# Performance work log

Measured on AMD Instinct MI355X. Metric: run time of the kernel, lower is better.

## Reference

```python
import jax, jax.numpy as jnp
import numpy as np

RANK = 32
ALPHA = 1.0
SCALE = ALPHA / RANK


def setup_inputs() -> dict:
    key = jax.random.key(0)
    k1, k2, k3, k4, k5 = jax.random.split(key, 5)
    B_, S, D_in, D_out = 4, 2048, 4096, 4096
    x = jax.random.normal(k1, (B_, S, D_in), dtype=jnp.float32)
    # nn.Linear weight: [out, in], kaiming-ish scale
    W = jax.random.normal(k2, (D_out, D_in), dtype=jnp.float32) / np.sqrt(D_in)
    bias = jax.random.normal(k3, (D_out,), dtype=jnp.float32) * 0.01
    A = jax.random.normal(k4, (D_in, RANK), dtype=jnp.float32) * 0.01
    # torch init is zeros for B; use small random so output depends on LoRA path
    Bm = jax.random.normal(k5, (RANK, D_out), dtype=jnp.float32) * 0.01
    return {"x": x, "W": W, "bias": bias, "A": A, "B": Bm}


def reference(x, W, bias, A, B):
    # Original: y = x @ (W + scale*(A@B)^T)^T + bias
    # Mathematically identical fused form (two GEMMs, no [in,out] delta):
    base = jnp.einsum('bsd,od->bso', x, W)          # [B,S,out]
    lora = jnp.einsum('bsr,ro->bso', x @ A, B)       # [B,S,rank]->[B,S,out]
    return base + SCALE * lora + bias
```

## Files before the change

kernel.cpp:

```cpp
#include <hip/hip_runtime.h>
#include <hip/hip_bf16.h>
#include <stdint.h>

#define RANK 32
#define SCALE (1.0f / 32.0f)

typedef __bf16 bf16x8 __attribute__((ext_vector_type(8)));
typedef float f32x4 __attribute__((ext_vector_type(4)));

__device__ __forceinline__ void gload16(const void* g, void* l) {
  __builtin_amdgcn_global_load_lds(
      (const __attribute__((address_space(1))) unsigned int*)g,
      (__attribute__((address_space(3))) unsigned int*)l, 16, 0, 0);
}

__device__ __forceinline__ unsigned short f2bf(float f) {
  __hip_bfloat16 h = __float2bfloat16(f);
  return *reinterpret_cast<unsigned short*>(&h);
}

__global__ __launch_bounds__(256) void transpose_B_k(const float* __restrict__ B,
                                                     float* __restrict__ Bt,
                                                     int Dout) {
  int idx = blockIdx.x * 256 + threadIdx.x;
  int r = idx / Dout;
  int o = idx - r * Dout;
  Bt[(long long)o * RANK + r] = B[idx];
}

__global__ __launch_bounds__(256) void merge_W_k(const float* __restrict__ W,
                                                 const float* __restrict__ A,
                                                 const float* __restrict__ Bt,
                                                 unsigned short* __restrict__ Wb,
                                                 int Din, int Dout) {
  __shared__ float sB[16 * RANK];
  int nib = Din / 256;
  int ib = blockIdx.x % nib;
  int ob = blockIdx.x / nib;
  int i0 = ib * 256, o0 = ob * 16;
  int t = threadIdx.x;

  if (t < 128) {
    reinterpret_cast<float4*>(sB)[t] =
        reinterpret_cast<const float4*>(Bt + (long long)o0 * RANK)[t];
  }

  float a[RANK];
  const float4* Ap = reinterpret_cast<const float4*>(A + (long long)(i0 + t) * RANK);
#pragma unroll
  for (int c = 0; c < RANK / 4; ++c) {
    float4 v = Ap[c];
    a[c * 4 + 0] = v.x; a[c * 4 + 1] = v.y;
    a[c * 4 + 2] = v.z; a[c * 4 + 3] = v.w;
  }
  __syncthreads();

  for (int o = 0; o < 16; ++o) {
    float d = 0.f;
#pragma unroll
    for (int j = 0; j < RANK; ++j) d += a[j] * sB[o * RANK + j];
    long long off = (long long)(o0 + o) * Din + i0 + t;
    Wb[off] = f2bf(W[off] + SCALE * d);
  }
}

__global__ __launch_bounds__(256) void cast_x_k(const float* __restrict__ in,
                                                unsigned short* __restrict__ out,
                                                long long n8) {
  long long i = (long long)blockIdx.x * 256 + threadIdx.x;
  if (i >= n8) return;
  const float4* in4 = reinterpret_cast<const float4*>(in) + i * 2;
  float4 v0 = in4[0], v1 = in4[1];
  union { unsigned short u[8]; uint4 q; } p;
  p.u[0] = f2bf(v0.x); p.u[1] = f2bf(v0.y); p.u[2] = f2bf(v0.z); p.u[3] = f2bf(v0.w);
  p.u[4] = f2bf(v1.x); p.u[5] = f2bf(v1.y); p.u[6] = f2bf(v1.z); p.u[7] = f2bf(v1.w);
  reinterpret_cast<uint4*>(out)[i] = p.q;
}

template <int NISSUE>
__device__ __forceinline__ void stage(const unsigned short* g, int K, int koff,
                                      int row0, unsigned short* ldsbase,
                                      int t, int wid) {
  int r = t >> 3;
  int cg = (t & 7) ^ (r & 7);
#pragma unroll
  for (int i = 0; i < NISSUE; ++i) {
    gload16(g + (long long)(row0 + i * 64 + r) * K + koff + cg * 8,
            ldsbase + (row0 + i * 64) * 64 + wid * 512);
  }
}

__device__ __forceinline__ int swz_off(int rowl, int k) {
  return rowl * 64 + ((((k) >> 3) ^ (rowl & 7)) << 3);
}

__global__ __launch_bounds__(512, 2) void gemm256_bias_k(
    const unsigned short* __restrict__ Xb,
    const unsigned short* __restrict__ Wb,
    const float* __restrict__ bias,
    float* __restrict__ Out,
    int M, int N, int K) {
  __shared__ unsigned short As[2][256 * 64];
  __shared__ unsigned short Bs[2][256 * 64];

  int nbn = N / 256;
  int cpx = gridDim.x >> 3;
  int bid = blockIdx.x;
  int swz = (bid & 7) * cpx + (bid >> 3);
  int bm = swz / nbn, bn = swz % nbn;

  int t = threadIdx.x;
  int wid = t >> 6, lane = t & 63;
  int wr = wid >> 2, wc = wid & 3;
  int lr = lane & 15, kq = (lane >> 4) * 8;
  int aw = wr * 128, bw = wc * 64;

  const unsigned short* ga = Xb + (long long)bm * 256 * K;
  const unsigned short* gb = Wb + (long long)bn * 256 * K;

  f32x4 acc[8][4] = {};
  bf16x8 a[4][2], b0[2][2], b0n[2][2], b1[2][2];

  const int NT = K / 64;

#define LDA(BUF, ROFF, MM, KS) \
  (*(const bf16x8*)&As[BUF][swz_off(aw + (ROFF) + (MM) * 16 + lr, (KS) * 32 + kq)])
#define LDB(BUF, ROFF, NN, KS) \
  (*(const bf16x8*)&Bs[BUF][swz_off(bw + (ROFF) + (NN) * 16 + lr, (KS) * 32 + kq)])

  stage<4>(ga, K, 0, 0, &As[0][0], t, wid);
  stage<4>(gb, K, 0, 0, &Bs[0][0], t, wid);
  stage<4>(ga, K, 64, 0, &As[1][0], t, wid);
  asm volatile("s_waitcnt vmcnt(4)" ::: "memory");
  __builtin_amdgcn_s_barrier();
#pragma unroll
  for (int m = 0; m < 4; ++m) {
    a[m][0] = LDA(0, 0, m, 0); a[m][1] = LDA(0, 0, m, 1);
  }
#pragma unroll
  for (int n = 0; n < 2; ++n) {
    b0[n][0] = LDB(0, 0, n, 0);  b0[n][1] = LDB(0, 0, n, 1);
    b1[n][0] = LDB(0, 32, n, 0); b1[n][1] = LDB(0, 32, n, 1);
  }

  for (int kt = 0; kt < NT; ++kt) {
    const int cur = kt & 1;
    int konext = (kt + 1) * 64, konext2 = (kt + 2) * 64;
    const bool hasN = (kt + 1 < NT);

    if (hasN) stage<2>(gb, K, konext, 0, &Bs[cur ^ 1][0], t, wid);
    __builtin_amdgcn_s_setprio(1);
#pragma unroll
    for (int m = 0; m < 4; ++m)
#pragma unroll
      for (int n = 0; n < 2; ++n)
#pragma unroll
        for (int ks = 0; ks < 2; ++ks)
          acc[m][n] = __builtin_amdgcn_mfma_f32_16x16x32_bf16(a[m][ks], b0[n][ks], acc[m][n], 0, 0, 0);
    __builtin_amdgcn_s_setprio(0);
    __builtin_amdgcn_s_barrier();

    if (hasN) stage<2>(gb, K, konext, 128, &Bs[cur ^ 1][0], t, wid);
    __builtin_amdgcn_s_setprio(1);
#pragma unroll
    for (int m = 0; m < 4; ++m) {
      acc[m][2] = __builtin_amdgcn_mfma_f32_16x16x32_bf16(a[m][0], b1[0][0], acc[m][2], 0, 0, 0);
      acc[m][2] = __builtin_amdgcn_mfma_f32_16x16x32_bf16(a[m][1], b1[0][1], acc[m][2], 0, 0, 0);
      acc[m][3] = __builtin_amdgcn_mfma_f32_16x16x32_bf16(a[m][0], b1[1][0], acc[m][3], 0, 0, 0);
      acc[m][3] = __builtin_amdgcn_mfma_f32_16x16x32_bf16(a[m][1], b1[1][1], acc[m][3], 0, 0, 0);
      a[m][0] = LDA(cur, 64, m, 0);
      a[m][1] = LDA(cur, 64, m, 1);
    }
    __builtin_amdgcn_s_setprio(0);
    __builtin_amdgcn_s_barrier();

    __builtin_amdgcn_s_setprio(1);
#pragma unroll
    for (int m = 0; m < 4; ++m)
#pragma unroll
      for (int n = 0; n < 2; ++n)
#pragma unroll
        for (int ks = 0; ks < 2; ++ks)
          acc[4 + m][2 + n] = __builtin_amdgcn_mfma_f32_16x16x32_bf16(a[m][ks], b1[n][ks], acc[4 + m][2 + n], 0, 0, 0);
    __builtin_amdgcn_s_setprio(0);
    __builtin_amdgcn_s_barrier();

    if (kt + 2 < NT) {
      stage<4>(ga, K, konext2, 0, &As[cur][0], t, wid);
      asm volatile("s_waitcnt vmcnt(4)" ::: "memory");
    } else if (hasN) {
      asm volatile("s_waitcnt vmcnt(0)" ::: "memory");
    }
    __builtin_amdgcn_s_barrier();

    if (hasN) {
      b0n[0][0] = LDB(cur ^ 1, 0, 0, 0); b0n[0][1] = LDB(cur ^ 1, 0, 0, 1);
      b0n[1][0] = LDB(cur ^ 1, 0, 1, 0); b0n[1][1] = LDB(cur ^ 1, 0, 1, 1);
    }
    __builtin_amdgcn_s_setprio(1);
#pragma unroll
    for (int m = 0; m < 4; ++m) {
      acc[4 + m][0] = __builtin_amdgcn_mfma_f32_16x16x32_bf16(a[m][0], b0[0][0], acc[4 + m][0], 0, 0, 0);
      acc[4 + m][0] = __builtin_amdgcn_mfma_f32_16x16x32_bf16(a[m][1], b0[0][1], acc[4 + m][0], 0, 0, 0);
      acc[4 + m][1] = __builtin_amdgcn_mfma_f32_16x16x32_bf16(a[m][0], b0[1][0], acc[4 + m][1], 0, 0, 0);
      acc[4 + m][1] = __builtin_amdgcn_mfma_f32_16x16x32_bf16(a[m][1], b0[1][1], acc[4 + m][1], 0, 0, 0);
      if (hasN) {
        a[m][0] = LDA(cur ^ 1, 0, m, 0);
        a[m][1] = LDA(cur ^ 1, 0, m, 1);
      }
    }
    __builtin_amdgcn_s_setprio(0);
    if (hasN) {
      b1[0][0] = LDB(cur ^ 1, 32, 0, 0); b1[0][1] = LDB(cur ^ 1, 32, 0, 1);
      b1[1][0] = LDB(cur ^ 1, 32, 1, 0); b1[1][1] = LDB(cur ^ 1, 32, 1, 1);
      b0[0][0] = b0n[0][0]; b0[0][1] = b0n[0][1];
      b0[1][0] = b0n[1][0]; b0[1][1] = b0n[1][1];
    }
    __builtin_amdgcn_s_barrier();
  }
#undef LDA
#undef LDB

  long long orow = (long long)bm * 256 + wr * 128;
  int ocol = bn * 256 + wc * 64;
#pragma unroll
  for (int n = 0; n < 4; ++n) {
    int gc = ocol + n * 16 + lr;
    float bv = bias[gc];
#pragma unroll
    for (int m = 0; m < 8; ++m) {
      long long gr = orow + m * 16 + (lane >> 4) * 4;
#pragma unroll
      for (int v = 0; v < 4; ++v)
        Out[(gr + v) * N + gc] = acc[m][n][v] + bv;
    }
  }
}

extern "C" void kernel_launch(void* const* d_in, const int* in_sizes, int n_in,
                              void* d_out, int out_size, void* d_ws, size_t ws_size,
                              hipStream_t stream) {
  const float* x    = (const float*)d_in[0];
  const float* W    = (const float*)d_in[1];
  const float* bias = (const float*)d_in[2];
  const float* A    = (const float*)d_in[3];
  const float* B    = (const float*)d_in[4];

  int Din  = in_sizes[3] / RANK;
  int Dout = in_sizes[4] / RANK;
  long long M = (long long)in_sizes[0] / Din;

  size_t xb_bytes = (size_t)M * Din * 2;
  size_t wb_bytes = (size_t)Dout * Din * 2;
  size_t bt_bytes = (size_t)Dout * RANK * 4;
  if (ws_size < xb_bytes + wb_bytes + bt_bytes) return;

  char* ws = (char*)d_ws;
  unsigned short* Xb = (unsigned short*)ws;
  unsigned short* Wb = (unsigned short*)(ws + xb_bytes);
  float* Bt          = (float*)(ws + xb_bytes + wb_bytes);

  transpose_B_k<<<dim3((Dout * RANK) / 256), dim3(256), 0, stream>>>(B, Bt, Dout);
  merge_W_k<<<dim3((Dout / 16) * (Din / 256)), dim3(256), 0, stream>>>(W, A, Bt, Wb, Din, Dout);
  long long n8 = M * Din / 8;
  cast_x_k<<<dim3((unsigned)(n8 / 256)), dim3(256), 0, stream>>>(x, Xb, n8);
  gemm256_bias_k<<<dim3((unsigned)((M / 256) * (Dout / 256))), dim3(512), 0, stream>>>(
      Xb, Wb, bias, (float*)d_out, (int)M, Dout, Din);
}
```

Before: 392.2 us.

## Restructure GEMM main loop into 8-phase quadrant schedule with interleaved staging

```diff
diff --git a/kernel.cpp b/kernel.cpp
--- a/kernel.cpp
+++ b/kernel.cpp
@@ -77,17 +77,15 @@
   reinterpret_cast<uint4*>(out)[i] = p.q;
 }
 
-template <int NISSUE>
-__device__ __forceinline__ void stage(const unsigned short* g, int K, int koff,
-                                      int row0, unsigned short* ldsbase,
-                                      int t, int wid) {
+__device__ __forceinline__ void stage2(const unsigned short* g, int K, int koff,
+                                       int row0, unsigned short* ldsreg,
+                                       int t, int wid) {
   int r = t >> 3;
   int cg = (t & 7) ^ (r & 7);
-#pragma unroll
-  for (int i = 0; i < NISSUE; ++i) {
-    gload16(g + (long long)(row0 + i * 64 + r) * K + koff + cg * 8,
-            ldsbase + (row0 + i * 64) * 64 + wid * 512);
-  }
+  gload16(g + (long long)(row0 + r) * K + koff + cg * 8,
+          ldsreg + row0 * 64 + wid * 512);
+  gload16(g + (long long)(row0 + 64 + r) * K + koff + cg * 8,
+          ldsreg + (row0 + 64) * 64 + wid * 512);
 }
 
 __device__ __forceinline__ int swz_off(int rowl, int k) {
@@ -113,123 +111,140 @@
   int wid = t >> 6, lane = t & 63;
   int wr = wid >> 2, wc = wid & 3;
   int lr = lane & 15, kq = (lane >> 4) * 8;
-  int aw = wr * 128, bw = wc * 64;
+  int wr64 = wr * 64, wc32 = wc * 32;
 
   const unsigned short* ga = Xb + (long long)bm * 256 * K;
   const unsigned short* gb = Wb + (long long)bn * 256 * K;
 
   f32x4 acc[8][4] = {};
-  bf16x8 a[4][2], b0[2][2], b0n[2][2], b1[2][2];
+  bf16x8 a[4][2], b0[2][2], b1[2][2];
 
   const int NT = K / 64;
-
-#define LDA(BUF, ROFF, MM, KS) \
-  (*(const bf16x8*)&As[BUF][swz_off(aw + (ROFF) + (MM) * 16 + lr, (KS) * 32 + kq)])
-#define LDB(BUF, ROFF, NN, KS) \
-  (*(const bf16x8*)&Bs[BUF][swz_off(bw + (ROFF) + (NN) * 16 + lr, (KS) * 32 + kq)])
-
-  stage<4>(ga, K, 0, 0, &As[0][0], t, wid);
-  stage<4>(gb, K, 0, 0, &Bs[0][0], t, wid);
-  stage<4>(ga, K, 64, 0, &As[1][0], t, wid);
-  asm volatile("s_waitcnt vmcnt(4)" ::: "memory");
+  const int iters = NT / 2;
+
+#define LDA(BUF, ROWBASE, KS) \
+  (*(const bf16x8*)&As[BUF][swz_off((ROWBASE) + lr, (KS) * 32 + kq)])
+#define LDB(BUF, ROWBASE, KS) \
+  (*(const bf16x8*)&Bs[BUF][swz_off((ROWBASE) + lr, (KS) * 32 + kq)])
+
+#define MFMA_Q(ACLUST, BCLUST, MOFF, NOFF)                                   \
+  __builtin_amdgcn_s_setprio(1);                                             \
+  _Pragma("unroll")                                                          \
+  for (int m = 0; m < 4; ++m)                                                \
+    _Pragma("unroll")                                                        \
+    for (int n = 0; n < 2; ++n)                                              \
+      _Pragma("unroll")                                                      \
+      for (int ks = 0; ks < 2; ++ks)                                         \
+        acc[(MOFF) + m][(NOFF) + n] = __builtin_amdgcn_mfma_f32_16x16x32_bf16(\
+            ACLUST[m][ks], BCLUST[n][ks], acc[(MOFF) + m][(NOFF) + n], 0, 0, 0); \
+  __builtin_amdgcn_s_setprio(0);
+
+  stage2(ga, K, 0, 0, &As[0][0], t, wid);
+  stage2(gb, K, 0, 0, &Bs[0][0], t, wid);
+  stage2(gb, K, 0, 128, &Bs[0][0], t, wid);
+  stage2(ga, K, 0, 128, &As[0][0], t, wid);
+  stage2(ga, K, 64, 0, &As[1][0], t, wid);
+  stage2(gb, K, 64, 0, &Bs[1][0], t, wid);
+  stage2(gb, K, 64, 128, &Bs[1][0], t, wid);
+  asm volatile("s_waitcnt vmcnt(6)" ::: "memory");
   __builtin_amdgcn_s_barrier();
-#pragma unroll
-  for (int m = 0; m < 4; ++m) {
-    a[m][0] = LDA(0, 0, m, 0); a[m][1] = LDA(0, 0, m, 1);
-  }
-#pragma unroll
-  for (int n = 0; n < 2; ++n) {
-    b0[n][0] = LDB(0, 0, n, 0);  b0[n][1] = LDB(0, 0, n, 1);
-    b1[n][0] = LDB(0, 32, n, 0); b1[n][1] = LDB(0, 32, n, 1);
-  }
-
-  for (int kt = 0; kt < NT; ++kt) {
-    const int cur = kt & 1;
-    int konext = (kt + 1) * 64, konext2 = (kt + 2) * 64;
-    const bool hasN = (kt + 1 < NT);
-
-    if (hasN) stage<2>(gb, K, konext, 0, &Bs[cur ^ 1][0], t, wid);
-    __builtin_amdgcn_s_setprio(1);
-#pragma unroll
-    for (int m = 0; m < 4; ++m)
-#pragma unroll
-      for (int n = 0; n < 2; ++n)
-#pragma unroll
-        for (int ks = 0; ks < 2; ++ks)
-          acc[m][n] = __builtin_amdgcn_mfma_f32_16x16x32_bf16(a[m][ks], b0[n][ks], acc[m][n], 0, 0, 0);
-    __builtin_amdgcn_s_setprio(0);
-    __builtin_amdgcn_s_barrier();
-
-    if (hasN) stage<2>(gb, K, konext, 128, &Bs[cur ^ 1][0], t, wid);
-    __builtin_amdgcn_s_setprio(1);
-#pragma unroll
-    for (int m = 0; m < 4; ++m) {
-      acc[m][2] = __builtin_amdgcn_mfma_f32_16x16x32_bf16(a[m][0], b1[0][0], acc[m][2], 0, 0, 0);
-      acc[m][2] = __builtin_amdgcn_mfma_f32_16x16x32_bf16(a[m][1], b1[0][1], acc[m][2], 0, 0, 0);
-      acc[m][3] = __builtin_amdgcn_mfma_f32_16x16x32_bf16(a[m][0], b1[1][0], acc[m][3], 0, 0, 0);
-      acc[m][3] = __builtin_amdgcn_mfma_f32_16x16x32_bf16(a[m][1], b1[1][1], acc[m][3], 0, 0, 0);
-      a[m][0] = LDA(cur, 64, m, 0);
-      a[m][1] = LDA(cur, 64, m, 1);
-    }
-    __builtin_amdgcn_s_setprio(0);
-    __builtin_amdgcn_s_barrier();
-
-    __builtin_amdgcn_s_setprio(1);
-#pragma unroll
-    for (int m = 0; m < 4; ++m)
-#pragma unroll
-      for (int n = 0; n < 2; ++n)
-#pragma unroll
-        for (int ks = 0; ks < 2; ++ks)
-          acc[4 + m][2 + n] = __builtin_amdgcn_mfma_f32_16x16x32_bf16(a[m][ks], b1[n][ks], acc[4 + m][2 + n], 0, 0, 0);
-    __builtin_amdgcn_s_setprio(0);
-    __builtin_amdgcn_s_barrier();
-
-    if (kt + 2 < NT) {
-      stage<4>(ga, K, konext2, 0, &As[cur][0], t, wid);
-      asm volatile("s_waitcnt vmcnt(4)" ::: "memory");
-    } else if (hasN) {
+
+  for (int j = 0; j < iters; ++j) {
+    const bool more = (j + 1 < iters);
+    int koY = (2 * j + 1) * 64, koX2 = koY + 64, koY2 = koX2 + 64;
+
+#pragma unroll
+    for (int m = 0; m < 4; ++m) {
+      a[m][0] = LDA(0, wr64 + m * 16, 0); a[m][1] = LDA(0, wr64 + m * 16, 1);
+    }
+#pragma unroll
+    for (int n = 0; n < 2; ++n) {
+      b0[n][0] = LDB(0, wc32 + n * 16, 0); b0[n][1] = LDB(0, wc32 + n * 16, 1);
+    }
+    stage2(ga, K, koY, 128, &As[1][0], t, wid);
+    __builtin_amdgcn_s_barrier();
+    MFMA_Q(a, b0, 0, 0)
+    __builtin_amdgcn_s_barrier();
+
+#pragma unroll
+    for (int n = 0; n < 2; ++n) {
+      b1[n][0] = LDB(0, 128 + wc32 + n * 16, 0); b1[n][1] = LDB(0, 128 + wc32 + n * 16, 1);
+    }
+    if (more) stage2(ga, K, koX2, 0, &As[0][0], t, wid);
+    __builtin_amdgcn_s_barrier();
+    MFMA_Q(a, b1, 0, 2)
+    __builtin_amdgcn_s_barrier();
+
+#pragma unroll
+    for (int m = 0; m < 4; ++m) {
+      a[m][0] = LDA(0, 128 + wr64 + m * 16, 0); a[m][1] = LDA(0, 128 + wr64 + m * 16, 1);
+    }
+    if (more) stage2(gb, K, koX2, 0, &Bs[0][0], t, wid);
+    __builtin_amdgcn_s_barrier();
+    MFMA_Q(a, b1, 4, 2)
+    __builtin_amdgcn_s_barrier();
+
+    if (more) {
+      stage2(gb, K, koX2, 128, &Bs[0][0], t, wid);
+      asm volatile("s_waitcnt vmcnt(6)" ::: "memory");
+    } else {
       asm volatile("s_waitcnt vmcnt(0)" ::: "memory");
     }
     __builtin_amdgcn_s_barrier();
-
-    if (hasN) {
-      b0n[0][0] = LDB(cur ^ 1, 0, 0, 0); b0n[0][1] = LDB(cur ^ 1, 0, 0, 1);
-      b0n[1][0] = LDB(cur ^ 1, 0, 1, 0); b0n[1][1] = LDB(cur ^ 1, 0, 1, 1);
-    }
-    __builtin_amdgcn_s_setprio(1);
-#pragma unroll
-    for (int m = 0; m < 4; ++m) {
-      acc[4 + m][0] = __builtin_amdgcn_mfma_f32_16x16x32_bf16(a[m][0], b0[0][0], acc[4 + m][0], 0, 0, 0);
-      acc[4 + m][0] = __builtin_amdgcn_mfma_f32_16x16x32_bf16(a[m][1], b0[0][1], acc[4 + m][0], 0, 0, 0);
-      acc[4 + m][1] = __builtin_amdgcn_mfma_f32_16x16x32_bf16(a[m][0], b0[1][0], acc[4 + m][1], 0, 0, 0);
-      acc[4 + m][1] = __builtin_amdgcn_mfma_f32_16x16x32_bf16(a[m][1], b0[1][1], acc[4 + m][1], 0, 0, 0);
-      if (hasN) {
-        a[m][0] = LDA(cur ^ 1, 0, m, 0);
-        a[m][1] = LDA(cur ^ 1, 0, m, 1);
-      }
-    }
-    __builtin_amdgcn_s_setprio(0);
-    if (hasN) {
-      b1[0][0] = LDB(cur ^ 1, 32, 0, 0); b1[0][1] = LDB(cur ^ 1, 32, 0, 1);
-      b1[1][0] = LDB(cur ^ 1, 32, 1, 0); b1[1][1] = LDB(cur ^ 1, 32, 1, 1);
-      b0[0][0] = b0n[0][0]; b0[0][1] = b0n[0][1];
-      b0[1][0] = b0n[1][0]; b0[1][1] = b0n[1][1];
-    }
+    MFMA_Q(a, b0, 4, 0)
+    __builtin_amdgcn_s_barrier();
+
+#pragma unroll
+    for (int m = 0; m < 4; ++m) {
+      a[m][0] = LDA(1, wr64 + m * 16, 0); a[m][1] = LDA(1, wr64 + m * 16, 1);
+    }
+#pragma unroll
+    for (int n = 0; n < 2; ++n) {
+      b0[n][0] = LDB(1, wc32 + n * 16, 0); b0[n][1] = LDB(1, wc32 + n * 16, 1);
+    }
+    if (more) stage2(ga, K, koX2, 128, &As[0][0], t, wid);
+    __builtin_amdgcn_s_barrier();
+    MFMA_Q(a, b0, 0, 0)
+    __builtin_amdgcn_s_barrier();
+
+#pragma unroll
+    for (int n = 0; n < 2; ++n) {
+      b1[n][0] = LDB(1, 128 + wc32 + n * 16, 0); b1[n][1] = LDB(1, 128 + wc32 + n * 16, 1);
+    }
+    if (more) stage2(ga, K, koY2, 0, &As[1][0], t, wid);
+    __builtin_amdgcn_s_barrier();
+    MFMA_Q(a, b1, 0, 2)
+    __builtin_amdgcn_s_barrier();
+
+#pragma unroll
+    for (int m = 0; m < 4; ++m) {
+      a[m][0] = LDA(1, 128 + wr64 + m * 16, 0); a[m][1] = LDA(1, 128 + wr64 + m * 16, 1);
+    }
+    if (more) stage2(gb, K, koY2, 0, &Bs[1][0], t, wid);
+    __builtin_amdgcn_s_barrier();
+    MFMA_Q(a, b1, 4, 2)
+    __builtin_amdgcn_s_barrier();
+
+    if (more) {
+      stage2(gb, K, koY2, 128, &Bs[1][0], t, wid);
+      asm volatile("s_waitcnt vmcnt(6)" ::: "memory");
+    }
+    __builtin_amdgcn_s_barrier();
+    MFMA_Q(a, b0, 4, 0)
     __builtin_amdgcn_s_barrier();
   }
 #undef LDA
 #undef LDB
-
-  long long orow = (long long)bm * 256 + wr * 128;
-  int ocol = bn * 256 + wc * 64;
+#undef MFMA_Q
+
+  int rq = (lane >> 4) * 4;
 #pragma unroll
   for (int n = 0; n < 4; ++n) {
-    int gc = ocol + n * 16 + lr;
+    int gc = bn * 256 + (n >= 2 ? 128 : 0) + wc32 + (n & 1) * 16 + lr;
     float bv = bias[gc];
 #pragma unroll
     for (int m = 0; m < 8; ++m) {
-      long long gr = orow + m * 16 + (lane >> 4) * 4;
+      long long gr = (long long)bm * 256 + (m >= 4 ? 128 : 0) + wr64 + (m & 3) * 16 + rq;
 #pragma unroll
       for (int v = 0; v < 4; ++v)
         Out[(gr + v) * N + gc] = acc[m][n][v] + bv;
```

Result: faster. 345.9 us (-11.8%).
